# Performance work log

Measured on AMD Instinct MI355X. Metric: run time of the kernel, lower is better.

## Reference

```python
import jax, jax.numpy as jnp
import numpy as np
from jax import lax

NUM_GROUP = 2048
GROUP_SIZE = 16


def setup_inputs() -> dict:
    key = jax.random.key(0)
    pcd = jax.random.normal(key, (4, 16384, 3), dtype=jnp.float32)
    return {"pcd": pcd}


def _fps(xyz, n_samples):
    # Furthest point sampling, matching CUDA FPS: start at index 0,
    # iteratively pick the point with max min-distance to the chosen set.
    B, N, _ = xyz.shape

    def step(carry, _):
        min_d, last = carry
        p = jnp.take_along_axis(xyz, last[:, None, None], axis=1)  # B,1,3
        d = jnp.sum((xyz - p) ** 2, axis=-1)                       # B,N
        min_d = jnp.minimum(min_d, d)
        nxt = jnp.argmax(min_d, axis=-1).astype(jnp.int32)         # B
        return (min_d, nxt), nxt

    first = jnp.zeros((B,), jnp.int32)
    init = (jnp.full((B, N), 1e10, xyz.dtype), first)
    _, rest = lax.scan(step, init, None, length=n_samples - 1)     # (n-1),B
    return jnp.concatenate([first[None, :], rest], axis=0).T       # B,n


def reference(pcd):
    xyz = pcd                                                      # channel==3 path
    B, N, _ = xyz.shape
    # centers via FPS + gather (N != num_group branch)
    fps_idx = _fps(xyz, NUM_GROUP)                                 # B,G
    center = jnp.take_along_axis(xyz, fps_idx[:, :, None], axis=1) # B,G,3
    # kNN of each center among all points (squared L2)
    d2 = (jnp.sum(center * center, -1)[:, :, None]
          - 2.0 * jnp.einsum('bgc,bnc->bgn', center, xyz)
          + jnp.sum(xyz * xyz, -1)[:, None, :])                    # B,G,N
    _, idx = lax.top_k(-d2, GROUP_SIZE)                            # B,G,M (nearest first)
    # gather neighborhoods per batch
    nbr = jax.vmap(lambda x, i: x[i])(xyz, idx)                    # B,G,M,3
    neighborhood = nbr - center[:, :, None, :]
    return neighborhood, center
```

## Files before the change

kernel.cpp:

```cpp
#include <hip/hip_runtime.h>
#include <math.h>


#pragma clang fp contract(off)

#define N_PTS 16384
#define N_GROUP 2048
#define GROUP_SIZE 16
#define FPS_THREADS 512
#define PPT (N_PTS / FPS_THREADS)
#define FPS_WAVES (FPS_THREADS / 64)
#define KNN_THREADS 256
#define KNN_WAVES (KNN_THREADS / 64)

__device__ __forceinline__ float fmul_sep(float a, float b) {
  float r = a * b;
  asm volatile("" : "+v"(r));
  return r;
}

__device__ __forceinline__ unsigned long long shfl_xor_u64(unsigned long long v, int off) {
  const unsigned int lo = __shfl_xor((unsigned int)v, off);
  const unsigned int hi = __shfl_xor((unsigned int)(v >> 32), off);
  return ((unsigned long long)hi << 32) | lo;
}

__global__ __launch_bounds__(FPS_THREADS, 2) void fps_kernel(
    const float* __restrict__ pcd, float* __restrict__ center) {
#pragma clang fp contract(off)
  const int b = blockIdx.x;
  const int t = threadIdx.x;
  const int lane = t & 63;
  const int wid = t >> 6;
  const float* xyz = pcd + (size_t)b * N_PTS * 3;
  const int base = t * PPT;

  float x[PPT], y[PPT], z[PPT], md[PPT];
#pragma unroll
  for (int i = 0; i < PPT; ++i) {
    const int idx = base + i;
    x[i] = xyz[idx * 3 + 0];
    y[i] = xyz[idx * 3 + 1];
    z[i] = xyz[idx * 3 + 2];
    md[i] = 1e10f;
  }

  float px = xyz[0], py = xyz[1], pz = xyz[2];
  if (t == 0) {
    center[((size_t)b * N_GROUP) * 3 + 0] = px;
    center[((size_t)b * N_GROUP) * 3 + 1] = py;
    center[((size_t)b * N_GROUP) * 3 + 2] = pz;
  }

  __shared__ unsigned long long skey[2][FPS_WAVES];
  __shared__ float sx[2][FPS_WAVES], sy[2][FPS_WAVES], sz[2][FPS_WAVES];

  for (int it = 1; it < N_GROUP; ++it) {
    const int p = it & 1;
    float bv = -1.0f;
    int bi = 0;
    float bx = 0.f, by = 0.f, bz = 0.f;
#pragma unroll
    for (int i = 0; i < PPT; ++i) {
      const float dx = x[i] - px;
      const float dy = y[i] - py;
      const float dz = z[i] - pz;
      const float d = (fmul_sep(dx, dx) + fmul_sep(dy, dy)) + fmul_sep(dz, dz);
      const float m = fminf(md[i], d);
      md[i] = m;
      if (m > bv) {
        bv = m; bi = base + i; bx = x[i]; by = y[i]; bz = z[i];
      }
    }
    unsigned long long key =
        ((unsigned long long)__float_as_uint(bv) << 32) |
        (unsigned int)(N_PTS - 1 - bi);

#pragma unroll
    for (int off = 32; off > 0; off >>= 1) {
      const unsigned long long ok = shfl_xor_u64(key, off);
      const float ox = __shfl_xor(bx, off);
      const float oy = __shfl_xor(by, off);
      const float oz = __shfl_xor(bz, off);
      if (ok > key) { key = ok; bx = ox; by = oy; bz = oz; }
    }
    if (lane == 0) {
      skey[p][wid] = key; sx[p][wid] = bx; sy[p][wid] = by; sz[p][wid] = bz;
    }
    __syncthreads();
    unsigned long long bk = skey[p][0];
    int bj = 0;
#pragma unroll
    for (int j = 1; j < FPS_WAVES; ++j) {
      const unsigned long long kj = skey[p][j];
      if (kj > bk) { bk = kj; bj = j; }
    }
    px = sx[p][bj]; py = sy[p][bj]; pz = sz[p][bj];
    if (t == 0) {
      center[((size_t)b * N_GROUP + it) * 3 + 0] = px;
      center[((size_t)b * N_GROUP + it) * 3 + 1] = py;
      center[((size_t)b * N_GROUP + it) * 3 + 2] = pz;
    }
  }
}

__global__ __launch_bounds__(KNN_THREADS) void knn_kernel(
    const float* __restrict__ pcd, const float* __restrict__ center,
    float* __restrict__ nbr) {
#pragma clang fp contract(off)
  const int lane = threadIdx.x & 63;
  const int gw = blockIdx.x * KNN_WAVES + (threadIdx.x >> 6);
  const int b = gw >> 11;
  const float* xyz = pcd + (size_t)b * N_PTS * 3;

  const float c0 = center[(size_t)gw * 3 + 0];
  const float c1 = center[(size_t)gw * 3 + 1];
  const float c2 = center[(size_t)gw * 3 + 2];
  const float cc = (fmul_sep(c0, c0) + fmul_sep(c1, c1)) + fmul_sep(c2, c2);

  float lval = INFINITY;
  int lidx = 0;
  float worst = INFINITY;

  for (int ch = 0; ch < N_PTS / 64; ++ch) {
    const int n = ch * 64 + lane;
    const float xp = xyz[n * 3 + 0];
    const float yp = xyz[n * 3 + 1];
    const float zp = xyz[n * 3 + 2];
    const float xx = (fmul_sep(xp, xp) + fmul_sep(yp, yp)) + fmul_sep(zp, zp);
    const float dot = fmaf(c2, zp, fmaf(c1, yp, c0 * xp));
    const float d2 = (cc - fmul_sep(2.0f, dot)) + xx;

    unsigned long long m = __ballot(d2 < worst);
    while (m) {
      const int srcl = __ffsll((unsigned long long)m) - 1;
      m &= (m - 1);
      const float nv = __shfl(d2, srcl);
      if (nv < worst) {
        const int ni = ch * 64 + srcl;
        const int rank = __popcll(__ballot(lane < GROUP_SIZE && lval <= nv));
        const float shv = __shfl_up(lval, 1);
        const int   shi = __shfl_up(lidx, 1);
        if (lane < GROUP_SIZE) {
          if (lane == rank)      { lval = nv;  lidx = ni;  }
          else if (lane > rank)  { lval = shv; lidx = shi; }
        }
        worst = __shfl(lval, 15);
      }
    }
  }

  if (lane < GROUP_SIZE) {
    const float ox = xyz[lidx * 3 + 0] - c0;
    const float oy = xyz[lidx * 3 + 1] - c1;
    const float oz = xyz[lidx * 3 + 2] - c2;
    const size_t o = ((size_t)gw * GROUP_SIZE + lane) * 3;
    nbr[o + 0] = ox; nbr[o + 1] = oy; nbr[o + 2] = oz;
  }
}

extern "C" void kernel_launch(void* const* d_in, const int* in_sizes, int n_in,
                              void* d_out, int out_size, void* d_ws, size_t ws_size,
                              hipStream_t stream) {
  const float* pcd = (const float*)d_in[0];
  const int B = in_sizes[0] / (N_PTS * 3);

  float* out = (float*)d_out;
  float* nbr = out;
  float* center = out + (size_t)B * N_GROUP * GROUP_SIZE * 3;

  fps_kernel<<<B, FPS_THREADS, 0, stream>>>(pcd, center);
  knn_kernel<<<(B * N_GROUP) / KNN_WAVES, KNN_THREADS, 0, stream>>>(pcd, center, nbr);
}
```

Before: 4.727 ms.

## Move FPS x/y coordinates to LDS and interleave point assignment across threads

```diff
diff --git a/kernel.cpp b/kernel.cpp
--- a/kernel.cpp
+++ b/kernel.cpp
@@ -25,25 +25,32 @@
   return ((unsigned long long)hi << 32) | lo;
 }
 
-__global__ __launch_bounds__(FPS_THREADS, 2) void fps_kernel(
-    const float* __restrict__ pcd, float* __restrict__ center) {
+__global__ __launch_bounds__(FPS_THREADS)
+__attribute__((amdgpu_waves_per_eu(2, 2)))
+void fps_kernel(const float* __restrict__ pcd, float* __restrict__ center) {
 #pragma clang fp contract(off)
   const int b = blockIdx.x;
   const int t = threadIdx.x;
   const int lane = t & 63;
   const int wid = t >> 6;
   const float* xyz = pcd + (size_t)b * N_PTS * 3;
-  const int base = t * PPT;
 
-  float x[PPT], y[PPT], z[PPT], md[PPT];
+  __shared__ float2 xy[N_PTS];
+  __shared__ unsigned long long skey[2][FPS_WAVES];
+  __shared__ float szw[2][FPS_WAVES];
+
+  float z[PPT], md[PPT];
 #pragma unroll
   for (int i = 0; i < PPT; ++i) {
-    const int idx = base + i;
-    x[i] = xyz[idx * 3 + 0];
-    y[i] = xyz[idx * 3 + 1];
+    const int idx = i * FPS_THREADS + t;
+    const float xv = xyz[idx * 3 + 0];
+    const float yv = xyz[idx * 3 + 1];
     z[i] = xyz[idx * 3 + 2];
+    xy[idx] = make_float2(xv, yv);
     md[i] = 1e10f;
   }
+#pragma unroll
+  for (int i = 0; i < PPT; ++i) asm("" : "+v"(z[i]));
 
   float px = xyz[0], py = xyz[1], pz = xyz[2];
   if (t == 0) {
@@ -51,26 +58,23 @@
     center[((size_t)b * N_GROUP) * 3 + 1] = py;
     center[((size_t)b * N_GROUP) * 3 + 2] = pz;
   }
-
-  __shared__ unsigned long long skey[2][FPS_WAVES];
-  __shared__ float sx[2][FPS_WAVES], sy[2][FPS_WAVES], sz[2][FPS_WAVES];
+  __syncthreads();
 
   for (int it = 1; it < N_GROUP; ++it) {
     const int p = it & 1;
     float bv = -1.0f;
     int bi = 0;
-    float bx = 0.f, by = 0.f, bz = 0.f;
+    float bz = 0.0f;
 #pragma unroll
     for (int i = 0; i < PPT; ++i) {
-      const float dx = x[i] - px;
-      const float dy = y[i] - py;
+      const float2 q = xy[i * FPS_THREADS + t];
+      const float dx = q.x - px;
+      const float dy = q.y - py;
       const float dz = z[i] - pz;
-      const float d = (fmul_sep(dx, dx) + fmul_sep(dy, dy)) + fmul_sep(dz, dz);
+      const float d = ((dx * dx) + (dy * dy)) + (dz * dz);
       const float m = fminf(md[i], d);
       md[i] = m;
-      if (m > bv) {
-        bv = m; bi = base + i; bx = x[i]; by = y[i]; bz = z[i];
-      }
+      if (m > bv) { bv = m; bi = i * FPS_THREADS + t; bz = z[i]; }
     }
     unsigned long long key =
         ((unsigned long long)__float_as_uint(bv) << 32) |
@@ -79,14 +83,10 @@
 #pragma unroll
     for (int off = 32; off > 0; off >>= 1) {
       const unsigned long long ok = shfl_xor_u64(key, off);
-      const float ox = __shfl_xor(bx, off);
-      const float oy = __shfl_xor(by, off);
       const float oz = __shfl_xor(bz, off);
-      if (ok > key) { key = ok; bx = ox; by = oy; bz = oz; }
+      if (ok > key) { key = ok; bz = oz; }
     }
-    if (lane == 0) {
-      skey[p][wid] = key; sx[p][wid] = bx; sy[p][wid] = by; sz[p][wid] = bz;
-    }
+    if (lane == 0) { skey[p][wid] = key; szw[p][wid] = bz; }
     __syncthreads();
     unsigned long long bk = skey[p][0];
     int bj = 0;
@@ -95,7 +95,9 @@
       const unsigned long long kj = skey[p][j];
       if (kj > bk) { bk = kj; bj = j; }
     }
-    px = sx[p][bj]; py = sy[p][bj]; pz = sz[p][bj];
+    const int kidx = N_PTS - 1 - (int)(unsigned int)(bk & 0xffffffffu);
+    const float2 pq = xy[kidx];
+    px = pq.x; py = pq.y; pz = szw[p][bj];
     if (t == 0) {
       center[((size_t)b * N_GROUP + it) * 3 + 0] = px;
       center[((size_t)b * N_GROUP + it) * 3 + 1] = py;
```

Measured after the change: 4.355 ms. -7.9%, faster.
